# Kernel optimization log

Measured on AMD Instinct MI355X. Metric: run time of the kernel, lower is better.

## Reference

```python
import jax, jax.numpy as jnp
import numpy as np
import math

N_NODES = 4096
DEG = 32
N_EDGES = N_NODES * DEG
H = 128
NUM_NODE_STATES = 4
NUM_EDGE_STATES = 4
NUM_GRAPHS = 64
UPPER_T, LOWER_T, NUM_ITERS, TEMP_EVAL = 1.0, 0.1, 10000, 0.1
TRAINING_STEP = 1000
NEG_INF = -1.0e9


def temp_by_step(step):
    # linear anneal upper->lower over NUM_ITERS; eval temp when step == -1
    if step == -1:
        return TEMP_EVAL
    frac = min(step / float(NUM_ITERS), 1.0)
    return UPPER_T + (LOWER_T - UPPER_T) * frac


def from_binary_states(bits):
    w = 2 ** jnp.arange(bits.shape[-1], dtype=jnp.int32)
    return jnp.sum(bits.astype(jnp.int32) * w, axis=-1)


def group_argmax_onehot(vals, group, num_segments):
    # gumbel_softmax(vals, group, tau=0, use_noise=False): one-hot argmax per group
    seg_max = jax.ops.segment_max(vals, group, num_segments=num_segments)
    return (vals >= seg_max[group]).astype(jnp.int32)


def layernorm(x, g, b, eps=1e-5):
    mu = jnp.mean(x, -1, keepdims=True)
    var = jnp.mean((x - mu) ** 2, -1, keepdims=True)
    return (x - mu) * jax.lax.rsqrt(var + eps) * g + b


def select_best(emb, bits, scalars, index, num_index):
    states = 2 * from_binary_states(bits)                  # even state codes
    group = states * num_index + index.astype(jnp.int32)   # unique (state, index) id
    best = group_argmax_onehot(-scalars[:, 0], group, emb.shape[0] * num_index)
    return emb[states + best]


def _forward(node_states, edge_states, scalars, edge_index, batch_vec,
             reverse_idx, edge_pos, training_step,
             emb_virtual, emb_reciever, emb_edge, emb_static,
             w_q, w_k, w_v, w_ek, w_ev, w_comb,
             ln_q_g, ln_q_b, ln_k_g, ln_k_b,
             tg_w1, tg_b1, tg_w2, tg_b2):
    src, dst = edge_index[0], edge_index[1]
    N = node_states.shape[0]
    E = src.shape[0]
    D = E // N  # uniform in-degree (incl. self loop)
    h = w_q.shape[0]

    # per-node scalars come from the self-loop edges (exactly one per node)
    loop_vals = jnp.where((src == dst)[:, None], scalars, 0.0)
    node_scalars = jax.ops.segment_sum(loop_vals, dst, num_segments=N)  # [N,1]

    node_fts = select_best(emb_virtual, node_states, node_scalars, batch_vec, NUM_GRAPHS)
    edge_fts = emb_edge[from_binary_states(edge_states)]

    Q = layernorm(node_fts @ w_q.T, ln_q_g, ln_q_b)
    K = layernorm(node_fts @ w_k.T, ln_k_g, ln_k_b)
    V = node_fts @ w_v.T

    # combined edge K/V
    sb = select_best(emb_reciever, node_states[src], scalars, dst, N)
    sender_s = node_scalars[src]
    reciever_s = node_scalars[dst]
    rlx = (scalars < reciever_s).astype(jnp.int32)
    rlx_d = ((sender_s + scalars) < reciever_s).astype(jnp.int32)
    static_fts = emb_static[(rlx + 2 * rlx_d)[:, 0]]
    combined = jnp.concatenate([edge_fts, edge_fts[reverse_idx], static_fts], axis=-1) @ w_comb.T
    edge_K = sb @ w_ek.T
    edge_V = combined @ w_ev.T

    # dense ragged batch per destination node (to_dense_batch equivalent)
    Kc = K[src] + edge_K
    Vc = V[src] + edge_V
    dense_K = jnp.zeros((N, D, h), Kc.dtype).at[dst, edge_pos].set(Kc)
    dense_V = jnp.zeros((N, D, h), Vc.dtype).at[dst, edge_pos].set(Vc)
    mask = jnp.zeros((N, D), bool).at[dst, edge_pos].set(True)

    logits = jnp.einsum('nh,ndh->nd', Q, dense_K) / math.sqrt(h)
    logits = jnp.where(mask, logits, NEG_INF)
    thr = jax.nn.relu(node_fts @ tg_w1.T + tg_b1) @ tg_w2.T + tg_b2  # [N,1]

    tau = temp_by_step(training_step)
    diff = logits - thr
    soft_mask = jax.nn.sigmoid(diff / tau)
    if training_step == -1:
        sel = (diff >= 0).astype(logits.dtype)
    else:
        beta = min(max(tau, 0.01), 1.0)
        sm = jnp.where(mask, jax.nn.softmax(logits, axis=-1), 0.0)
        hard = (diff >= 0).astype(logits.dtype)
        proxy = (1.0 - beta) * soft_mask + beta * sm
        sel = jax.lax.stop_gradient(hard - proxy) + proxy  # straight-through
    sel = sel * mask.astype(logits.dtype)

    msg = jnp.einsum('nd,ndh->nh', sel, dense_V)  # sum aggregation (attention='hard')
    node_out = node_fts + msg
    edge_out = edge_fts + msg[dst]
    return node_out, edge_out


def _build_graph():
    # ring graph, uniform degree DEG per destination incl. self loop;
    # offsets symmetric so every edge has a reverse edge; dst-sorted.
    offs = [0]
    for k in range(1, DEG // 2):
        offs += [k, -k]
    offs.append(N_NODES // 2)  # self-reverse offset
    offs = np.asarray(offs)
    offs_mod = offs % N_NODES
    rev_t = np.array([int(np.where(offs_mod == ((-o) % N_NODES))[0][0]) for o in offs])
    t = np.tile(np.arange(DEG), N_NODES)
    dst = np.repeat(np.arange(N_NODES), DEG)
    src = (dst + offs[t]) % N_NODES
    reverse_idx = src * DEG + rev_t[t]
    return src, dst, reverse_idx, t


def setup_inputs():
    key = jax.random.key(0)
    ks = jax.random.split(key, 20)
    src, dst, reverse_idx, pos = _build_graph()
    s = 1.0 / math.sqrt(H)
    return {
        "node_states": jax.random.randint(ks[0], (N_NODES, NUM_NODE_STATES), 0, 2, dtype=jnp.int32),
        "edge_states": jax.random.randint(ks[1], (N_EDGES, NUM_EDGE_STATES), 0, 2, dtype=jnp.int32),
        "scalars": jax.random.normal(ks[2], (N_EDGES, 1), jnp.float32),
        "edge_index": jnp.asarray(np.stack([src, dst]), dtype=jnp.int32),
        "batch_vec": jnp.asarray(np.arange(N_NODES) // (N_NODES // NUM_GRAPHS), dtype=jnp.int32),
        "reverse_idx": jnp.asarray(reverse_idx, dtype=jnp.int32),
        "edge_pos": jnp.asarray(pos, dtype=jnp.int32),
        "training_step": TRAINING_STEP,
        "emb_virtual": 0.05 * jax.random.normal(ks[3], (2 ** (NUM_NODE_STATES + 1), H), jnp.float32),
        "emb_reciever": 0.05 * jax.random.normal(ks[4], (2 ** (NUM_NODE_STATES + 1), H), jnp.float32),
        "emb_edge": 0.05 * jax.random.normal(ks[5], (2 ** NUM_EDGE_STATES, H), jnp.float32),
        "emb_static": 0.05 * jax.random.normal(ks[6], (4, H), jnp.float32),
        "w_q": s * jax.random.normal(ks[7], (H, H), jnp.float32),
        "w_k": s * jax.random.normal(ks[8], (H, H), jnp.float32),
        "w_v": s * jax.random.normal(ks[9], (H, H), jnp.float32),
        "w_ek": s * jax.random.normal(ks[10], (H, H), jnp.float32),
        "w_ev": s * jax.random.normal(ks[11], (H, H), jnp.float32),
        "w_comb": s * jax.random.normal(ks[12], (H, 3 * H), jnp.float32),
        "ln_q_g": jnp.ones((H,), jnp.float32),
        "ln_q_b": jnp.zeros((H,), jnp.float32),
        "ln_k_g": jnp.ones((H,), jnp.float32),
        "ln_k_b": jnp.zeros((H,), jnp.float32),
        "tg_w1": s * jax.random.normal(ks[13], (H, H), jnp.float32),
        "tg_b1": jnp.zeros((H,), jnp.float32),
        "tg_w2": s * jax.random.normal(ks[14], (1, H), jnp.float32),
        "tg_b2": jnp.full((1,), -5.0, jnp.float32),
    }


def reference(node_states, edge_states, scalars, edge_index, batch_vec,
              reverse_idx, edge_pos, training_step,
              emb_virtual, emb_reciever, emb_edge, emb_static,
              w_q, w_k, w_v, w_ek, w_ev, w_comb,
              ln_q_g, ln_q_b, ln_k_g, ln_k_b,
              tg_w1, tg_b1, tg_w2, tg_b2):
    return _forward(node_states, edge_states, scalars, edge_index, batch_vec,
                    reverse_idx, edge_pos, training_step,
                    emb_virtual, emb_reciever, emb_edge, emb_static,
                    w_q, w_k, w_v, w_ek, w_ev, w_comb,
                    ln_q_g, ln_q_b, ln_k_g, ln_k_b,
                    tg_w1, tg_b1, tg_w2, tg_b2)
```

## Files before the change

### kernel.cpp

```cpp
#include <hip/hip_runtime.h>

#define N_NODES 4096
#define DEG 32
#define N_EDGES (N_NODES * DEG)
#define H 128
#define NUM_GRAPHS 64

#define WS_SEG_NODE 0
#define WS_SINT     2048
#define WS_QEMB     6144
#define WS_KEMB     10240
#define WS_EK       14336
#define WS_VEMB     18432
#define WS_EV1      22528
#define WS_EV2      24576
#define WS_EV3      26624
#define WS_THR      27136
#define WS_QK32     27168
#define WS_QEK32    28192

#define SM_V     0
#define SM_E1    4096
#define SM_E2    6144
#define SM_E3    8192
#define SM_EMB   8704
#define SM_QK    10752
#define SM_QEK   11776
#define SM_THR   12800
#define SM_QSH   12832
#define SM_SB16  12840
#define SM_TOTAL 12968

__device__ __forceinline__ unsigned int fkey(float x) {
    unsigned int u = __float_as_uint(x);
    return (u & 0x80000000u) ? ~u : (u | 0x80000000u);
}
__device__ __forceinline__ float funkey(unsigned int k) {
    unsigned int u = (k & 0x80000000u) ? (k & 0x7FFFFFFFu) : ~k;
    return __uint_as_float(u);
}
__device__ __forceinline__ int frombin4(const int* __restrict__ p) {
    int4 q = *(const int4*)p;
    return q.x + (q.y << 1) + (q.z << 2) + (q.w << 3);
}
__device__ __forceinline__ int edge_off(int p) {
    return (p == 0) ? 0 : (p == 31 ? 2048 : ((p & 1) ? ((p + 1) >> 1) : -(p >> 1)));
}
__device__ __forceinline__ int rev_pos(int p) {
    return (p == 0) ? 0 : (p == 31 ? 31 : ((p & 1) ? p + 1 : p - 1));
}
__device__ __forceinline__ float dot128(const float* __restrict__ a, const float* __restrict__ b) {
    float s = 0.f;
#pragma unroll
    for (int k = 0; k < 128; k += 4) {
        float4 av = *(const float4*)(a + k);
        float4 bv = *(const float4*)(b + k);
        s += av.x * bv.x + av.y * bv.y + av.z * bv.z + av.w * bv.w;
    }
    return s;
}

__device__ __forceinline__ float ln256(float v, int t, const float* __restrict__ g,
                                       const float* __restrict__ bb, float* red) {
    int h = t & 127;
    red[t] = v;
    __syncthreads();
    for (int off = 64; off > 0; off >>= 1) {
        if (h < off) red[t] += red[t + off];
        __syncthreads();
    }
    float mu = red[t & 128] / 128.f;
    __syncthreads();
    float c = v - mu;
    red[t] = c * c;
    __syncthreads();
    for (int off = 64; off > 0; off >>= 1) {
        if (h < off) red[t] += red[t + off];
        __syncthreads();
    }
    float var = red[t & 128] / 128.f;
    return c * rsqrtf(var + 1e-5f) * g[h] + bb[h];
}

__global__ __launch_bounds__(256) void kA(
    const int* __restrict__ node_states, const float* __restrict__ scalars,
    const float* __restrict__ emb_virtual, const float* __restrict__ emb_reciever,
    const float* __restrict__ emb_edge, const float* __restrict__ emb_static,
    const float* __restrict__ w_q, const float* __restrict__ w_k,
    const float* __restrict__ w_v, const float* __restrict__ w_ek,
    const float* __restrict__ w_ev, const float* __restrict__ w_comb,
    const float* __restrict__ ln_q_g, const float* __restrict__ ln_q_b,
    const float* __restrict__ ln_k_g, const float* __restrict__ ln_k_b,
    const float* __restrict__ tg_w1, const float* __restrict__ tg_b1,
    const float* __restrict__ tg_w2, const float* __restrict__ tg_b2,
    float* __restrict__ ws) {
    __shared__ float red[256];
    int b = blockIdx.x, t = threadIdx.x;
    unsigned int* wsu = (unsigned int*)ws;
    if (b < 98) {
        int j = 2 * b + (t >> 7), tt = t & 127;
        if (j < 32) {
            float v = dot128(emb_virtual + j * H, w_q + tt * H);
            ws[WS_QEMB + j * H + tt] = ln256(v, t, ln_q_g, ln_q_b, red);
        } else if (j < 64) {
            int s = j - 32;
            float v = dot128(emb_virtual + s * H, w_k + tt * H);
            ws[WS_KEMB + s * H + tt] = ln256(v, t, ln_k_g, ln_k_b, red);
        } else if (j < 96) {
            int s = j - 64;
            ws[WS_VEMB + s * H + tt] = dot128(emb_virtual + s * H, w_v + tt * H);
        } else if (j < 128) {
            int s = j - 96;
            ws[WS_EK + s * H + tt] = dot128(emb_reciever + s * H, w_ek + tt * H);
        } else if (j < 160) {
            int s = j - 128;
            float hval = fmaxf(dot128(emb_virtual + s * H, tg_w1 + tt * H) + tg_b1[tt], 0.f);
            red[t] = hval * tg_w2[tt];
            __syncthreads();
            for (int off = 64; off > 0; off >>= 1) {
                if (tt < off) red[t] += red[t + off];
                __syncthreads();
            }
            if (tt == 0) ws[WS_THR + s] = red[t & 128] + tg_b2[0];
        } else {
            int r = j - 160;
            float cv;
            if (r < 16)
                cv = dot128(emb_edge + r * H, w_comb + tt * 384);
            else if (r < 32)
                cv = dot128(emb_edge + (r - 16) * H, w_comb + tt * 384 + 128);
            else
                cv = dot128(emb_static + (r - 32) * H, w_comb + tt * 384 + 256);
            red[t] = cv;
            __syncthreads();
            float ev = dot128(red + (t & 128), w_ev + tt * H);
            if (r < 16)
                ws[WS_EV1 + r * H + tt] = ev;
            else if (r < 32)
                ws[WS_EV2 + (r - 16) * H + tt] = ev;
            else
                ws[WS_EV3 + (r - 32) * H + tt] = ev;
        }
    } else {
        __shared__ unsigned arr[64];
        int b2 = b - 98;
        int n = b2 * 256 + t;
        int si = frombin4(node_states + n * 4);
        wsu[WS_SINT + n] = (unsigned)si;
        float nsum = scalars[n * DEG];
        if (t < 64) arr[t] = 0u;
        __syncthreads();
        atomicMax(&arr[(t >> 6) * 16 + si], fkey(-nsum));
        __syncthreads();
        if (t < 64) {
            int gl = t >> 4, ssi = t & 15;
            wsu[WS_SEG_NODE + 2 * ssi * NUM_GRAPHS + (b2 * 4 + gl)] = arr[gl * 16 + ssi];
        }
    }
}

__global__ __launch_bounds__(256) void kB(float* __restrict__ ws) {
    int idx = blockIdx.x * 256 + threadIdx.x;
    int tab = idx >> 10;
    int r = (idx >> 5) & 31, c = idx & 31;
    const float* qrow = ws + WS_QEMB + r * H;
    const float* krow = ws + (tab ? WS_EK : WS_KEMB) + c * H;
    ws[WS_QK32 + idx] = dot128(qrow, krow);
}

__global__ __launch_bounds__(256) void kC(
    const int* __restrict__ edge_states, const float* __restrict__ scalars,
    const int* __restrict__ training_step, const float* __restrict__ emb_virtual,
    const float* __restrict__ emb_edge, const float* __restrict__ ws,
    float* __restrict__ node_out, float* __restrict__ edge_out) {
    __shared__ __align__(16) float sm[SM_TOTAL];
    unsigned* smu = (unsigned*)sm;
    int* smi = (int*)sm;
    const unsigned int* wsu = (const unsigned int*)ws;
    int tid = threadIdx.x, blk = blockIdx.x;

    if (tid < 128) smu[SM_SB16 + tid] = 0u;
    {
        float4* s4 = (float4*)sm;
        const float4* w4 = (const float4*)ws;
        const float4* ee4 = (const float4*)emb_edge;
        for (int i = tid; i < 1024; i += 256) s4[SM_V / 4 + i] = w4[WS_VEMB / 4 + i];
        for (int i = tid; i < 512; i += 256) {
            s4[SM_E1 / 4 + i] = w4[WS_EV1 / 4 + i];
            s4[SM_E2 / 4 + i] = w4[WS_EV2 / 4 + i];
            s4[SM_EMB / 4 + i] = ee4[i];
            s4[SM_QK / 4 + i] = w4[WS_QK32 / 4 + i];
        }
        if (tid < 128) s4[SM_E3 / 4 + tid] = w4[WS_EV3 / 4 + tid];
        if (tid >= 128 && tid < 136) s4[SM_THR / 4 + (tid - 128)] = w4[WS_THR / 4 + (tid - 128)];
    }
    if (tid < 8) {
        int n0 = blk * 8 + tid;
        int sd = (int)wsu[WS_SINT + n0];
        float ns_d0 = scalars[n0 * DEG];
        int q = 2 * sd +
                ((-ns_d0 >= funkey(wsu[WS_SEG_NODE + 2 * sd * NUM_GRAPHS + (n0 >> 6)]))
                     ? 1
                     : 0);
        smi[SM_QSH + tid] = q;
    }

    int g = tid >> 5, lane = tid & 31;
    int n = blk * 8 + g;
    int e = blk * 256 + tid;
    int p = lane;
    int s = (n + edge_off(p) + N_NODES) & (N_NODES - 1);
    int re = s * DEG + rev_pos(p);
    float sc = scalars[e];
    int ss = (int)wsu[WS_SINT + s];
    float ns_s = scalars[s * DEG], ns_d = scalars[n * DEG];
    int a = 2 * ss +
            ((-ns_s >= funkey(wsu[WS_SEG_NODE + 2 * ss * NUM_GRAPHS + (s >> 6)])) ? 1 : 0);
    int st = ((sc < ns_d) ? 1 : 0) + 2 * ((ns_s + sc < ns_d) ? 1 : 0);
    int es_e = frombin4(edge_states + e * 4);
    int es_r = frombin4(edge_states + re * 4);
    __syncthreads();
    atomicMax(&smu[SM_SB16 + g * 16 + ss], fkey(-sc));
    __syncthreads();

    int qn = smi[SM_QSH + g];
    int sbi = 2 * ss + ((-sc >= funkey(smu[SM_SB16 + g * 16 + ss])) ? 1 : 0);
    float logit =
        (sm[SM_QK + qn * 32 + a] + sm[SM_QEK + qn * 32 + sbi]) * 0.08838834764831845f;
    float thr = sm[SM_THR + qn];
    float mx = logit;
#pragma unroll
    for (int off = 16; off > 0; off >>= 1) mx = fmaxf(mx, __shfl_xor(mx, off, 32));
    float ex = __expf(logit - mx);
    float sum = ex;
#pragma unroll
    for (int off = 16; off > 0; off >>= 1) sum += __shfl_xor(sum, off, 32);
    float sm_ = ex / sum;
    float diff = logit - thr;
    float hard = (diff >= 0.f) ? 1.f : 0.f;
    int step = training_step[0];
    float sel;
    if (step == -1) {
        sel = hard;
    } else {
        float tau = 1.0f + (0.1f - 1.0f) * fminf((float)step / 10000.0f, 1.0f);
        float beta = fminf(fmaxf(tau, 0.01f), 1.0f);
        float soft = 1.f / (1.f + __expf(-diff / tau));
        float proxy = (1.f - beta) * soft + beta * sm_;
        sel = (hard - proxy) + proxy;
    }
    unsigned vsh =
        (unsigned)a | ((unsigned)es_e << 5) | ((unsigned)es_r << 9) | ((unsigned)st << 13);

    float4 msg = make_float4(0.f, 0.f, 0.f, 0.f);
#pragma unroll 8
    for (int s2 = 0; s2 < 32; ++s2) {
        float w = __shfl(sel, s2, 32);
        unsigned v = (unsigned)__shfl((int)vsh, s2, 32);
        float4 rv = ((const float4*)(sm + SM_V + (v & 31) * H))[lane];
        float4 r1 = ((const float4*)(sm + SM_E1 + ((v >> 5) & 15) * H))[lane];
        float4 r2 = ((const float4*)(sm + SM_E2 + ((v >> 9) & 15) * H))[lane];
        float4 r3 = ((const float4*)(sm + SM_E3 + ((v >> 13) & 3) * H))[lane];
        msg.x += w * (rv.x + r1.x + r2.x + r3.x);
        msg.y += w * (rv.y + r1.y + r2.y + r3.y);
        msg.z += w * (rv.z + r1.z + r2.z + r3.z);
        msg.w += w * (rv.w + r1.w + r2.w + r3.w);
    }
    {
        float4 ev = ((const float4*)(emb_virtual + qn * H))[lane];
        float4 r;
        r.x = ev.x + msg.x;
        r.y = ev.y + msg.y;
        r.z = ev.z + msg.z;
        r.w = ev.w + msg.w;
        ((float4*)node_out)[n * 32 + lane] = r;
    }

    {
        float4* eo = (float4*)edge_out;
        size_t ebase = ((size_t)blk * 256 + (size_t)g * 32) * 32 + (size_t)lane;
#pragma unroll 8
        for (int ed = 0; ed < 32; ++ed) {
            unsigned v = (unsigned)__shfl((int)vsh, ed, 32);
            int b4 = (v >> 5) & 15;
            float4 em = ((const float4*)(sm + SM_EMB + b4 * H))[lane];
            float4 r;
            r.x = em.x + msg.x;
            r.y = em.y + msg.y;
            r.z = em.z + msg.z;
            r.w = em.w + msg.w;
            eo[ebase + (size_t)ed * 32] = r;
        }
    }
}

extern "C" void kernel_launch(void* const* d_in, const int* in_sizes, int n_in,
                              void* d_out, int out_size, void* d_ws, size_t ws_size,
                              hipStream_t stream) {
    (void)in_sizes; (void)n_in; (void)out_size; (void)ws_size;
    const int* node_states = (const int*)d_in[0];
    const int* edge_states = (const int*)d_in[1];
    const float* scalars = (const float*)d_in[2];
    const int* training_step = (const int*)d_in[7];
    const float* emb_virtual = (const float*)d_in[8];
    const float* emb_reciever = (const float*)d_in[9];
    const float* emb_edge = (const float*)d_in[10];
    const float* emb_static = (const float*)d_in[11];
    const float* w_q = (const float*)d_in[12];
    const float* w_k = (const float*)d_in[13];
    const float* w_v = (const float*)d_in[14];
    const float* w_ek = (const float*)d_in[15];
    const float* w_ev = (const float*)d_in[16];
    const float* w_comb = (const float*)d_in[17];
    const float* ln_q_g = (const float*)d_in[18];
    const float* ln_q_b = (const float*)d_in[19];
    const float* ln_k_g = (const float*)d_in[20];
    const float* ln_k_b = (const float*)d_in[21];
    const float* tg_w1 = (const float*)d_in[22];
    const float* tg_b1 = (const float*)d_in[23];
    const float* tg_w2 = (const float*)d_in[24];
    const float* tg_b2 = (const float*)d_in[25];

    float* ws = (float*)d_ws;
    float* node_out = (float*)d_out;
    float* edge_out = node_out + (size_t)N_NODES * H;

    kA<<<114, 256, 0, stream>>>(node_states, scalars, emb_virtual, emb_reciever,
                                emb_edge, emb_static, w_q, w_k, w_v, w_ek, w_ev, w_comb,
                                ln_q_g, ln_q_b, ln_k_g, ln_k_b, tg_w1, tg_b1, tg_w2,
                                tg_b2, ws);
    kB<<<8, 256, 0, stream>>>(ws);
    kC<<<N_NODES / 8, 256, 0, stream>>>(edge_states, scalars, training_step,
                                        emb_virtual, emb_edge, ws, node_out, edge_out);
}
```

Baseline: 153.7 us.

## Bin per-edge weights by table index before summing embedding rows

Each edge's selection weight is now accumulated through shared-memory atomics into per-node bins, one bin per row of the value tables (32 V rows, 16+16 edge rows, 4 static rows). The node message is then a dense 68-row weighted sum instead of 32 edges times 4 gathered rows. Shared memory is repacked so the tables sit contiguously and load with a single copy loop, and edge states are passed through shared memory instead of shuffles. This adds LDS float atomics and an extra barrier, and changes summation order slightly.

New measurement: 157.8 us. 1.03x slower.

```diff
diff --git a/kernel.cpp b/kernel.cpp
--- a/kernel.cpp
+++ b/kernel.cpp
@@ -20,16 +20,15 @@
 #define WS_QEK32    28192
 
 #define SM_V     0
-#define SM_E1    4096
-#define SM_E2    6144
-#define SM_E3    8192
 #define SM_EMB   8704
-#define SM_QK    10752
-#define SM_QEK   11776
-#define SM_THR   12800
+#define SM_THR   10752
+#define SM_QK    10784
+#define SM_QEK   11808
 #define SM_QSH   12832
 #define SM_SB16  12840
-#define SM_TOTAL 12968
+#define SM_BINS  12968
+#define SM_VSH   13512
+#define SM_TOTAL 13768
 
 __device__ __forceinline__ unsigned int fkey(float x) {
     unsigned int u = __float_as_uint(x);
@@ -179,20 +178,15 @@
     const unsigned int* wsu = (const unsigned int*)ws;
     int tid = threadIdx.x, blk = blockIdx.x;
 
+    for (int i = tid; i < 544; i += 256) sm[SM_BINS + i] = 0.f;
     if (tid < 128) smu[SM_SB16 + tid] = 0u;
     {
         float4* s4 = (float4*)sm;
         const float4* w4 = (const float4*)ws;
         const float4* ee4 = (const float4*)emb_edge;
-        for (int i = tid; i < 1024; i += 256) s4[SM_V / 4 + i] = w4[WS_VEMB / 4 + i];
-        for (int i = tid; i < 512; i += 256) {
-            s4[SM_E1 / 4 + i] = w4[WS_EV1 / 4 + i];
-            s4[SM_E2 / 4 + i] = w4[WS_EV2 / 4 + i];
-            s4[SM_EMB / 4 + i] = ee4[i];
-            s4[SM_QK / 4 + i] = w4[WS_QK32 / 4 + i];
-        }
-        if (tid < 128) s4[SM_E3 / 4 + tid] = w4[WS_EV3 / 4 + tid];
-        if (tid >= 128 && tid < 136) s4[SM_THR / 4 + (tid - 128)] = w4[WS_THR / 4 + (tid - 128)];
+        for (int i = tid; i < 2176; i += 256) s4[i] = w4[WS_VEMB / 4 + i];
+        for (int i = tid; i < 512; i += 256) s4[SM_EMB / 4 + i] = ee4[i];
+        for (int i = tid; i < 520; i += 256) s4[SM_THR / 4 + i] = w4[WS_THR / 4 + i];
     }
     if (tid < 8) {
         int n0 = blk * 8 + tid;
@@ -249,24 +243,31 @@
         float proxy = (1.f - beta) * soft + beta * sm_;
         sel = (hard - proxy) + proxy;
     }
-    unsigned vsh =
-        (unsigned)a | ((unsigned)es_e << 5) | ((unsigned)es_r << 9) | ((unsigned)st << 13);
+    {
+        float* wb = sm + SM_BINS + g * 68;
+        atomicAdd(wb + a, sel);
+        atomicAdd(wb + 32 + es_e, sel);
+        atomicAdd(wb + 48 + es_r, sel);
+        atomicAdd(wb + 64 + st, sel);
+    }
+    smu[SM_VSH + tid] = (unsigned)es_e;
+    __syncthreads();
 
     float4 msg = make_float4(0.f, 0.f, 0.f, 0.f);
-#pragma unroll 8
-    for (int s2 = 0; s2 < 32; ++s2) {
-        float w = __shfl(sel, s2, 32);
-        unsigned v = (unsigned)__shfl((int)vsh, s2, 32);
-        float4 rv = ((const float4*)(sm + SM_V + (v & 31) * H))[lane];
-        float4 r1 = ((const float4*)(sm + SM_E1 + ((v >> 5) & 15) * H))[lane];
-        float4 r2 = ((const float4*)(sm + SM_E2 + ((v >> 9) & 15) * H))[lane];
-        float4 r3 = ((const float4*)(sm + SM_E3 + ((v >> 13) & 3) * H))[lane];
-        msg.x += w * (rv.x + r1.x + r2.x + r3.x);
-        msg.y += w * (rv.y + r1.y + r2.y + r3.y);
-        msg.z += w * (rv.z + r1.z + r2.z + r3.z);
-        msg.w += w * (rv.w + r1.w + r2.w + r3.w);
-    }
     {
+        const float* wb = sm + SM_BINS + g * 68;
+#pragma unroll
+        for (int bb = 0; bb < 68; bb += 4) {
+            float4 wq = *(const float4*)(wb + bb);
+            float4 r0 = ((const float4*)(sm + (bb + 0) * H))[lane];
+            float4 r1 = ((const float4*)(sm + (bb + 1) * H))[lane];
+            float4 r2 = ((const float4*)(sm + (bb + 2) * H))[lane];
+            float4 r3 = ((const float4*)(sm + (bb + 3) * H))[lane];
+            msg.x += wq.x * r0.x + wq.y * r1.x + wq.z * r2.x + wq.w * r3.x;
+            msg.y += wq.x * r0.y + wq.y * r1.y + wq.z * r2.y + wq.w * r3.y;
+            msg.z += wq.x * r0.z + wq.y * r1.z + wq.z * r2.z + wq.w * r3.z;
+            msg.w += wq.x * r0.w + wq.y * r1.w + wq.z * r2.w + wq.w * r3.w;
+        }
         float4 ev = ((const float4*)(emb_virtual + qn * H))[lane];
         float4 r;
         r.x = ev.x + msg.x;
@@ -281,8 +282,7 @@
         size_t ebase = ((size_t)blk * 256 + (size_t)g * 32) * 32 + (size_t)lane;
 #pragma unroll 8
         for (int ed = 0; ed < 32; ++ed) {
-            unsigned v = (unsigned)__shfl((int)vsh, ed, 32);
-            int b4 = (v >> 5) & 15;
+            int b4 = (int)smu[SM_VSH + g * 32 + ed];
             float4 em = ((const float4*)(sm + SM_EMB + b4 * H))[lane];
             float4 r;
             r.x = em.x + msg.x;
```
